# Performance work log

Hardware: AMD Instinct MI355X
Metric: run time of the kernel (lower is better)

The kernel has to match this reference:

```python
import jax, jax.numpy as jnp
import numpy as np

B = 64
L_IN = 4001
L_CONV = 998  # (4001-10)//4 + 1
D = 1000
EPS = 1e-5


def _convlin(x, cw, cb, lw, lb):
    # x: (B,1,4001), cw: (1,1,10), lw: (1000,998)
    y = jax.lax.conv_general_dilated(
        x, cw, window_strides=(4,), padding='VALID',
        dimension_numbers=('NCH', 'OIH', 'NCH')) + cb[None, :, None]  # (B,1,998)
    y = y @ lw.T + lb  # (B,1,1000)
    return jax.nn.relu(y)


def setup_inputs() -> dict:
    key = jax.random.key(0)
    ks = jax.random.split(key, 24)
    f32 = jnp.float32
    inp = {
        'x': jax.random.normal(ks[0], (B, 1, L_IN), dtype=f32),
        'bn_gamma': jnp.ones((L_IN,), f32),
        'bn_beta': jnp.zeros((L_IN,), f32),
        'bn_mean': jax.random.normal(ks[1], (L_IN,), f32) * 0.1,
        'bn_var': jax.random.uniform(ks[2], (L_IN,), f32, 0.5, 1.5),
        'conv_w_q': jax.random.normal(ks[3], (1, 1, 10), f32) * 0.3,
        'conv_b_q': jax.random.normal(ks[4], (1,), f32) * 0.1,
        'lin_w_q': jax.random.normal(ks[5], (D, L_CONV), f32) * (1.0 / np.sqrt(L_CONV)),
        'lin_b_q': jax.random.normal(ks[6], (D,), f32) * 0.02,
        'conv_w_k': jax.random.normal(ks[7], (1, 1, 10), f32) * 0.3,
        'conv_b_k': jax.random.normal(ks[8], (1,), f32) * 0.1,
        'lin_w_k': jax.random.normal(ks[9], (D, L_CONV), f32) * (1.0 / np.sqrt(L_CONV)),
        'lin_b_k': jax.random.normal(ks[10], (D,), f32) * 0.02,
        'conv_w_v': jax.random.normal(ks[11], (1, 1, 10), f32) * 0.3,
        'conv_b_v': jax.random.normal(ks[12], (1,), f32) * 0.1,
        'lin_w_v': jax.random.normal(ks[13], (D, L_CONV), f32) * (1.0 / np.sqrt(L_CONV)),
        'lin_b_v': jax.random.normal(ks[14], (D,), f32) * 0.02,
        'in_proj_w': jax.random.normal(ks[15], (3, 1), f32),
        'in_proj_b': jax.random.normal(ks[16], (3,), f32) * 0.02,
        'out_proj_w': jax.random.normal(ks[17], (1, 1), f32),
        'out_proj_b': jax.random.normal(ks[18], (1,), f32) * 0.02,
        'out_w': jax.random.normal(ks[19], (D, D), f32) * (1.0 / np.sqrt(D)),
        'out_b': jax.random.normal(ks[20], (D,), f32) * 0.02,
    }
    return inp


def reference(x, bn_gamma, bn_beta, bn_mean, bn_var,
              conv_w_q, conv_b_q, lin_w_q, lin_b_q,
              conv_w_k, conv_b_k, lin_w_k, lin_b_k,
              conv_w_v, conv_b_v, lin_w_v, lin_b_v,
              in_proj_w, in_proj_b, out_proj_w, out_proj_b,
              out_w, out_b):
    # BatchNorm1d over last dim (eval mode, running stats); x: (B,1,4001)
    xn = (x - bn_mean[None, None, :]) * jax.lax.rsqrt(bn_var[None, None, :] + EPS)
    xn = xn * bn_gamma[None, None, :] + bn_beta[None, None, :]

    Q = _convlin(xn, conv_w_q, conv_b_q, lin_w_q, lin_b_q)[:, 0, :]  # (B,1000)
    K = _convlin(xn, conv_w_k, conv_b_k, lin_w_k, lin_b_k)[:, 0, :]
    V = _convlin(xn, conv_w_v, conv_b_v, lin_w_v, lin_b_v)[:, 0, :]

    # MHA with embed_dim=1, num_heads=1 -> scalar in-projections, scale = 1
    q = Q * in_proj_w[0, 0] + in_proj_b[0]  # (B,1000)
    k = K * in_proj_w[1, 0] + in_proj_b[1]
    v = V * in_proj_w[2, 0] + in_proj_b[2]

    scores = q[:, :, None] * k[:, None, :]  # (B,1000,1000)
    attn = jax.nn.softmax(scores, axis=-1)
    ctx = jnp.einsum('bqk,bk->bq', attn, v)  # (B,1000)
    ctx = ctx * out_proj_w[0, 0] + out_proj_b[0]

    out = ctx[:, None, :] @ out_w.T + out_b  # (B,1,1000)
    return out
```

## Files before the change

kernel.cpp:

```cpp
#include <hip/hip_runtime.h>
#include <math.h>

#define NB 64
#define LIN 4001
#define LC 998
#define ND 1000
#define EPSBN 1e-5f

#define CKL 100
#define NCHL 10
#define CKO 96
#define NCHO 11

#define OFF_CONVT 0u
#define OFF_PP    191616u
#define OFF_CF    2157696u
#define OFF_OP    2221696u

__global__ __launch_bounds__(256) void k_bnconv(
    const float* __restrict__ x,
    const float* __restrict__ g, const float* __restrict__ be,
    const float* __restrict__ mu, const float* __restrict__ va,
    const float* __restrict__ cwq, const float* __restrict__ cbq,
    const float* __restrict__ cwk, const float* __restrict__ cbk,
    const float* __restrict__ cwv, const float* __restrict__ cbv,
    float* __restrict__ convT)
{
    int j = blockIdx.x * 256 + threadIdx.x;
    int b = blockIdx.y;
    if (j >= LC) return;
    const float* xb = x + (size_t)b * LIN + 4 * j;
    float aq = 0.f, ak = 0.f, av = 0.f;
#pragma unroll
    for (int t = 0; t < 10; ++t) {
        int i = 4 * j + t;
        float s  = g[i] * rsqrtf(va[i] + EPSBN);
        float xn = (xb[t] - mu[i]) * s + be[i];
        aq = fmaf(xn, cwq[t], aq);
        ak = fmaf(xn, cwk[t], ak);
        av = fmaf(xn, cwv[t], av);
    }
    convT[((size_t)0 * LC + j) * 64 + b] = aq + cbq[0];
    convT[((size_t)1 * LC + j) * 64 + b] = ak + cbk[0];
    convT[((size_t)2 * LC + j) * 64 + b] = av + cbv[0];
}

template <int CKT>
__device__ __forceinline__ void gemm_tile(
    const float* __restrict__ Asrc,
    const float* __restrict__ Brow,
    int ldB, int dgb, int j0, int jc,
    float* __restrict__ Pt,
    float* lds)
{
    constexpr int LDW = CKT + 1;
    constexpr int F2R = CKT / 2;
    float* ldsC = lds;
    float* ldsW = lds + CKT * 64;
    int tid  = threadIdx.x;
    int lane = tid & 63;
    int w    = tid >> 6;
    int b0   = (lane & 7) << 3;
    int d0   = (lane >> 3) << 3;

    {
        const float4* src = (const float4*)Asrc;
        float4* dst = (float4*)ldsC;
        int n = jc * 16;
        for (int t = tid; t < n; t += 256) dst[t] = src[t];
    }
    for (int idx = tid; idx < 64 * F2R; idx += 256) {
        int dd = idx / F2R, j2 = idx % F2R;
        int dg = dgb + dd;
        float2 v = make_float2(0.f, 0.f);
        if (dg < ND && 2 * j2 < jc)
            v = *(const float2*)(Brow + (size_t)dg * ldB + j0 + 2 * j2);
        ldsW[dd * LDW + 2 * j2]     = v.x;
        ldsW[dd * LDW + 2 * j2 + 1] = v.y;
    }
    __syncthreads();

    float acc[8][8];
#pragma unroll
    for (int i = 0; i < 8; ++i)
#pragma unroll
        for (int jx = 0; jx < 8; ++jx) acc[i][jx] = 0.f;

    int js = (jc * w) >> 2;
    int je = (jc * (w + 1)) >> 2;
#pragma unroll 2
    for (int jj = js; jj < je; ++jj) {
        float4 c0 = *(const float4*)(ldsC + jj * 64 + b0);
        float4 c1 = *(const float4*)(ldsC + jj * 64 + b0 + 4);
        float cv[8] = {c0.x, c0.y, c0.z, c0.w, c1.x, c1.y, c1.z, c1.w};
        float wv[8];
#pragma unroll
        for (int r = 0; r < 8; ++r) wv[r] = ldsW[(d0 + r) * LDW + jj];
#pragma unroll
        for (int i = 0; i < 8; ++i)
#pragma unroll
            for (int jx = 0; jx < 8; ++jx)
                acc[i][jx] = fmaf(cv[i], wv[jx], acc[i][jx]);
    }
    __syncthreads();

    for (int p = 0; p < 2; ++p) {
        float* red = lds + w * 2304;
#pragma unroll
        for (int i = 0; i < 8; ++i)
            *(float4*)(red + (b0 + i) * 36 + (d0 >> 1)) =
                make_float4(acc[i][4*p], acc[i][4*p+1], acc[i][4*p+2], acc[i][4*p+3]);
        __syncthreads();
        for (int t = tid; t < 512; t += 256) {
            int bb = t >> 3, gg = t & 7;
            int o = bb * 36 + 4 * gg;
            float4 a0 = *(const float4*)(lds + o);
            float4 a1 = *(const float4*)(lds + 2304 + o);
            float4 a2 = *(const float4*)(lds + 4608 + o);
            float4 a3 = *(const float4*)(lds + 6912 + o);
            float4 s;
            s.x = a0.x + a1.x + a2.x + a3.x;
            s.y = a0.y + a1.y + a2.y + a3.y;
            s.z = a0.z + a1.z + a2.z + a3.z;
            s.w = a0.w + a1.w + a2.w + a3.w;
            *(float4*)(Pt + bb * 64 + 8 * gg + 4 * p) = s;
        }
        __syncthreads();
    }
}

__global__ __launch_bounds__(256) void k_lin(
    const float* __restrict__ convT,
    const float* __restrict__ lwq, const float* __restrict__ lwk,
    const float* __restrict__ lwv,
    float* __restrict__ Pp)
{
    __shared__ float lds[12864];
    int dgb   = blockIdx.x * 64;
    int which = blockIdx.y;
    int chunk = blockIdx.z;
    int j0 = chunk * CKL;
    int jc = (LC - j0 < CKL) ? (LC - j0) : CKL;
    const float* lw = (which == 0) ? lwq : ((which == 1) ? lwk : lwv);
    const float* Asrc = convT + ((size_t)which * LC + j0) * 64;
    float* Pt = Pp + (((size_t)chunk * 3 + which) * 16 + blockIdx.x) * 4096;
    gemm_tile<CKL>(Asrc, lw, LC, dgb, j0, jc, Pt, lds);
}

__global__ __launch_bounds__(256) void k_actattn(
    const float* __restrict__ Pp,
    const float* __restrict__ lbq, const float* __restrict__ lbk,
    const float* __restrict__ lbv,
    const float* __restrict__ ipw, const float* __restrict__ ipb,
    const float* __restrict__ opw, const float* __restrict__ opb,
    float* __restrict__ cfT)
{
    __shared__ float ldsKV[2048];
    __shared__ float rmax[4];
    __shared__ float rmin[4];
    int tid = threadIdx.x;
    int iq  = blockIdx.x;
    int b   = blockIdx.y;
    int w   = tid >> 6;

    for (int i = tid; i < ND; i += 256) {
        int ig  = i >> 6;
        int off = (i & 63) | (b << 6);
        float s1 = 0.f, s2 = 0.f;
#pragma unroll
        for (int c = 0; c < NCHL; ++c) {
            size_t base = (((size_t)c * 3 + 1) * 16 + ig) * 4096 + off;
            s1 += Pp[base];
            s2 += Pp[base + 16 * 4096];
        }
        ldsKV[2 * i]     = fmaxf(s1 + lbk[i], 0.f) * ipw[1] + ipb[1];
        ldsKV[2 * i + 1] = fmaxf(s2 + lbv[i], 0.f) * ipw[2] + ipb[2];
    }
    int  i   = iq * 250 + tid;
    bool act = (tid < 250);
    float qi = 0.f;
    if (act) {
        int ig  = i >> 6;
        int off = (i & 63) | (b << 6);
        float s0 = 0.f;
#pragma unroll
        for (int c = 0; c < NCHL; ++c)
            s0 += Pp[(((size_t)c * 3) * 16 + ig) * 4096 + off];
        qi = fmaxf(s0 + lbq[i], 0.f) * ipw[0] + ipb[0];
    }
    __syncthreads();

    const float2* kv2 = (const float2*)ldsKV;
    float km = -INFINITY, kn = INFINITY;
    for (int idx = tid; idx < ND; idx += 256) {
        float2 f = kv2[idx];
        km = fmaxf(km, f.x);
        kn = fminf(kn, f.x);
    }
#pragma unroll
    for (int off = 1; off < 64; off <<= 1) {
        km = fmaxf(km, __shfl_xor(km, off));
        kn = fminf(kn, __shfl_xor(kn, off));
    }
    if ((tid & 63) == 0) { rmax[w] = km; rmin[w] = kn; }
    __syncthreads();
    km = fmaxf(fmaxf(rmax[0], rmax[1]), fmaxf(rmax[2], rmax[3]));
    kn = fminf(fminf(rmin[0], rmin[1]), fminf(rmin[2], rmin[3]));

    float m = (qi >= 0.f) ? qi * km : qi * kn;
    float den = 0.f, num = 0.f;
#pragma unroll 4
    for (int j = 0; j < ND; ++j) {
        float2 f = kv2[j];
        float e  = __expf(fmaf(qi, f.x, -m));
        den += e;
        num = fmaf(e, f.y, num);
    }
    if (act)
        cfT[(size_t)i * 64 + b] = (num / den) * opw[0] + opb[0];
}

__global__ __launch_bounds__(256) void k_out(
    const float* __restrict__ cfT, const float* __restrict__ W,
    float* __restrict__ Op)
{
    __shared__ float lds[12352];
    int egb   = blockIdx.x * 64;
    int chunk = blockIdx.y;
    int j0 = chunk * CKO;
    int jc = (ND - j0 < CKO) ? (ND - j0) : CKO;
    const float* Asrc = cfT + (size_t)j0 * 64;
    float* Pt = Op + ((size_t)chunk * 16 + blockIdx.x) * 4096;
    gemm_tile<CKO>(Asrc, W, ND, egb, j0, jc, Pt, lds);
}

__global__ __launch_bounds__(256) void k_fin(
    const float* __restrict__ Op, const float* __restrict__ outb,
    float* __restrict__ out)
{
    int e = blockIdx.x * 256 + threadIdx.x;
    int b = blockIdx.y;
    if (e >= ND) return;
    float s = outb[e];
    size_t cell = ((size_t)(e >> 6)) * 4096 + (b << 6) + (e & 63);
    for (int c = 0; c < NCHO; ++c)
        s += Op[(size_t)c * 16 * 4096 + cell];
    out[(size_t)b * ND + e] = s;
}

extern "C" void kernel_launch(void* const* d_in, const int* in_sizes, int n_in,
                              void* d_out, int out_size, void* d_ws, size_t ws_size,
                              hipStream_t stream)
{
    const float* x    = (const float*)d_in[0];
    const float* g    = (const float*)d_in[1];
    const float* be   = (const float*)d_in[2];
    const float* mu   = (const float*)d_in[3];
    const float* va   = (const float*)d_in[4];
    const float* cwq  = (const float*)d_in[5];
    const float* cbq  = (const float*)d_in[6];
    const float* lwq  = (const float*)d_in[7];
    const float* lbq  = (const float*)d_in[8];
    const float* cwk  = (const float*)d_in[9];
    const float* cbk  = (const float*)d_in[10];
    const float* lwk  = (const float*)d_in[11];
    const float* lbk  = (const float*)d_in[12];
    const float* cwv  = (const float*)d_in[13];
    const float* cbv  = (const float*)d_in[14];
    const float* lwv  = (const float*)d_in[15];
    const float* lbv  = (const float*)d_in[16];
    const float* ipw  = (const float*)d_in[17];
    const float* ipb  = (const float*)d_in[18];
    const float* opw  = (const float*)d_in[19];
    const float* opb  = (const float*)d_in[20];
    const float* W    = (const float*)d_in[21];
    const float* outb = (const float*)d_in[22];

    float* ws    = (float*)d_ws;
    float* convT = ws + OFF_CONVT;
    float* Pp    = ws + OFF_PP;
    float* cfT   = ws + OFF_CF;
    float* Op    = ws + OFF_OP;
    float* out   = (float*)d_out;

    k_bnconv <<<dim3(4, 64), 256, 0, stream>>>(x, g, be, mu, va,
                                               cwq, cbq, cwk, cbk, cwv, cbv, convT);
    k_lin    <<<dim3(16, 3, NCHL), 256, 0, stream>>>(convT, lwq, lwk, lwv, Pp);
    k_actattn<<<dim3(4, 64), 256, 0, stream>>>(Pp, lbq, lbk, lbv,
                                               ipw, ipb, opw, opb, cfT);
    k_out    <<<dim3(16, NCHO), 256, 0, stream>>>(cfT, W, Op);
    k_fin    <<<dim3(4, 64), 256, 0, stream>>>(Op, outb, out);
}
```

Baseline: 178.1 us.

## Replace split-K partial buffers with atomic accumulation and drop final reduction kernel

```diff
diff --git a/kernel.cpp b/kernel.cpp
--- a/kernel.cpp
+++ b/kernel.cpp
@@ -9,13 +9,13 @@
 
 #define CKL 100
 #define NCHL 10
-#define CKO 96
-#define NCHO 11
+#define CKO 50
+#define NCHO 20
 
 #define OFF_CONVT 0u
-#define OFF_PP    191616u
-#define OFF_CF    2157696u
-#define OFF_OP    2221696u
+#define OFF_Q     191616u
+#define OFF_KV    255616u
+#define OFF_CF    386688u
 
 __global__ __launch_bounds__(256) void k_bnconv(
     const float* __restrict__ x,
@@ -24,25 +24,39 @@
     const float* __restrict__ cwq, const float* __restrict__ cbq,
     const float* __restrict__ cwk, const float* __restrict__ cbk,
     const float* __restrict__ cwv, const float* __restrict__ cbv,
-    float* __restrict__ convT)
-{
-    int j = blockIdx.x * 256 + threadIdx.x;
-    int b = blockIdx.y;
-    if (j >= LC) return;
-    const float* xb = x + (size_t)b * LIN + 4 * j;
-    float aq = 0.f, ak = 0.f, av = 0.f;
-#pragma unroll
-    for (int t = 0; t < 10; ++t) {
-        int i = 4 * j + t;
-        float s  = g[i] * rsqrtf(va[i] + EPSBN);
-        float xn = (xb[t] - mu[i]) * s + be[i];
-        aq = fmaf(xn, cwq[t], aq);
-        ak = fmaf(xn, cwk[t], ak);
-        av = fmaf(xn, cwv[t], av);
-    }
-    convT[((size_t)0 * LC + j) * 64 + b] = aq + cbq[0];
-    convT[((size_t)1 * LC + j) * 64 + b] = ak + cbk[0];
-    convT[((size_t)2 * LC + j) * 64 + b] = av + cbv[0];
+    const float* __restrict__ lbq, const float* __restrict__ lbk,
+    const float* __restrict__ lbv, const float* __restrict__ outb,
+    float* __restrict__ convT,
+    float* __restrict__ q, float* __restrict__ kv, float* __restrict__ out)
+{
+    int tid = threadIdx.x;
+    int jt  = blockIdx.x;
+    int b   = blockIdx.y;
+
+    if (tid < 250) {
+        int e = jt * 250 + tid;
+        q[(size_t)b * ND + e] = lbq[e];
+        *(float2*)&kv[(size_t)b * 2048 + 2 * e] = make_float2(lbk[e], lbv[e]);
+        out[(size_t)b * ND + e] = outb[e];
+    }
+
+    int j = jt * 256 + tid;
+    if (j < LC) {
+        const float* xb = x + (size_t)b * LIN + 4 * j;
+        float aq = 0.f, ak = 0.f, av = 0.f;
+#pragma unroll
+        for (int t = 0; t < 10; ++t) {
+            int i = 4 * j + t;
+            float s  = g[i] * rsqrtf(va[i] + EPSBN);
+            float xn = (xb[t] - mu[i]) * s + be[i];
+            aq = fmaf(xn, cwq[t], aq);
+            ak = fmaf(xn, cwk[t], ak);
+            av = fmaf(xn, cwv[t], av);
+        }
+        convT[((size_t)0 * LC + j) * 64 + b] = aq + cbq[0];
+        convT[((size_t)1 * LC + j) * 64 + b] = ak + cbk[0];
+        convT[((size_t)2 * LC + j) * 64 + b] = av + cbv[0];
+    }
 }
 
 template <int CKT>
@@ -50,7 +64,7 @@
     const float* __restrict__ Asrc,
     const float* __restrict__ Brow,
     int ldB, int dgb, int j0, int jc,
-    float* __restrict__ Pt,
+    float* __restrict__ obase, int rowst, int cstr, int coff,
     float* lds)
 {
     constexpr int LDW = CKT + 1;
@@ -88,7 +102,6 @@
 
     int js = (jc * w) >> 2;
     int je = (jc * (w + 1)) >> 2;
-#pragma unroll 2
     for (int jj = js; jj < je; ++jj) {
         float4 c0 = *(const float4*)(ldsC + jj * 64 + b0);
         float4 c1 = *(const float4*)(ldsC + jj * 64 + b0 + 4);
@@ -123,7 +136,12 @@
             s.y = a0.y + a1.y + a2.y + a3.y;
             s.z = a0.z + a1.z + a2.z + a3.z;
             s.w = a0.w + a1.w + a2.w + a3.w;
-            *(float4*)(Pt + bb * 64 + 8 * gg + 4 * p) = s;
+            int col = dgb + 8 * gg + 4 * p;
+            float* row = obase + (size_t)bb * rowst;
+            if (col     < ND) atomicAdd(row + (size_t)(col    ) * cstr + coff, s.x);
+            if (col + 1 < ND) atomicAdd(row + (size_t)(col + 1) * cstr + coff, s.y);
+            if (col + 2 < ND) atomicAdd(row + (size_t)(col + 2) * cstr + coff, s.z);
+            if (col + 3 < ND) atomicAdd(row + (size_t)(col + 3) * cstr + coff, s.w);
         }
         __syncthreads();
     }
@@ -133,60 +151,48 @@
     const float* __restrict__ convT,
     const float* __restrict__ lwq, const float* __restrict__ lwk,
     const float* __restrict__ lwv,
-    float* __restrict__ Pp)
+    float* __restrict__ q, float* __restrict__ kv)
 {
     __shared__ float lds[12864];
-    int dgb   = blockIdx.x * 64;
+    int dgx   = blockIdx.x;
     int which = blockIdx.y;
     int chunk = blockIdx.z;
     int j0 = chunk * CKL;
     int jc = (LC - j0 < CKL) ? (LC - j0) : CKL;
     const float* lw = (which == 0) ? lwq : ((which == 1) ? lwk : lwv);
     const float* Asrc = convT + ((size_t)which * LC + j0) * 64;
-    float* Pt = Pp + (((size_t)chunk * 3 + which) * 16 + blockIdx.x) * 4096;
-    gemm_tile<CKL>(Asrc, lw, LC, dgb, j0, jc, Pt, lds);
-}
-
-__global__ __launch_bounds__(256) void k_actattn(
-    const float* __restrict__ Pp,
-    const float* __restrict__ lbq, const float* __restrict__ lbk,
-    const float* __restrict__ lbv,
+    float* obase; int rowst, cstr, coff;
+    if (which == 0) { obase = q;  rowst = ND;   cstr = 1; coff = 0; }
+    else            { obase = kv; rowst = 2048; cstr = 2; coff = which - 1; }
+    gemm_tile<CKL>(Asrc, lw, LC, dgx * 64, j0, jc, obase, rowst, cstr, coff, lds);
+}
+
+__global__ __launch_bounds__(256) void k_attn(
+    const float* __restrict__ q, const float* __restrict__ kv,
     const float* __restrict__ ipw, const float* __restrict__ ipb,
     const float* __restrict__ opw, const float* __restrict__ opb,
     float* __restrict__ cfT)
 {
     __shared__ float ldsKV[2048];
+    __shared__ float sden[256];
+    __shared__ float snum[256];
     __shared__ float rmax[4];
     __shared__ float rmin[4];
     int tid = threadIdx.x;
-    int iq  = blockIdx.x;
     int b   = blockIdx.y;
     int w   = tid >> 6;
-
-    for (int i = tid; i < ND; i += 256) {
-        int ig  = i >> 6;
-        int off = (i & 63) | (b << 6);
-        float s1 = 0.f, s2 = 0.f;
-#pragma unroll
-        for (int c = 0; c < NCHL; ++c) {
-            size_t base = (((size_t)c * 3 + 1) * 16 + ig) * 4096 + off;
-            s1 += Pp[base];
-            s2 += Pp[base + 16 * 4096];
+    int ii  = tid & 63;
+    int i   = blockIdx.x * 64 + ii;
+
+    {
+        const float2* src = (const float2*)(kv + (size_t)b * 2048);
+        float2* dst = (float2*)ldsKV;
+        float w1 = ipw[1], b1 = ipb[1], w2 = ipw[2], b2 = ipb[2];
+        for (int t = tid; t < 1024; t += 256) {
+            float2 rv = src[t];
+            dst[t] = make_float2(fmaf(fmaxf(rv.x, 0.f), w1, b1),
+                                 fmaf(fmaxf(rv.y, 0.f), w2, b2));
         }
-        ldsKV[2 * i]     = fmaxf(s1 + lbk[i], 0.f) * ipw[1] + ipb[1];
-        ldsKV[2 * i + 1] = fmaxf(s2 + lbv[i], 0.f) * ipw[2] + ipb[2];
-    }
-    int  i   = iq * 250 + tid;
-    bool act = (tid < 250);
-    float qi = 0.f;
-    if (act) {
-        int ig  = i >> 6;
-        int off = (i & 63) | (b << 6);
-        float s0 = 0.f;
-#pragma unroll
-        for (int c = 0; c < NCHL; ++c)
-            s0 += Pp[(((size_t)c * 3) * 16 + ig) * 4096 + off];
-        qi = fmaxf(s0 + lbq[i], 0.f) * ipw[0] + ipb[0];
     }
     __syncthreads();
 
@@ -202,50 +208,46 @@
         km = fmaxf(km, __shfl_xor(km, off));
         kn = fminf(kn, __shfl_xor(kn, off));
     }
-    if ((tid & 63) == 0) { rmax[w] = km; rmin[w] = kn; }
+    if (ii == 0) { rmax[w] = km; rmin[w] = kn; }
     __syncthreads();
     km = fmaxf(fmaxf(rmax[0], rmax[1]), fmaxf(rmax[2], rmax[3]));
     kn = fminf(fminf(rmin[0], rmin[1]), fminf(rmin[2], rmin[3]));
 
+    float qi = 0.f;
+    if (i < ND)
+        qi = fmaf(fmaxf(q[(size_t)b * ND + i], 0.f), ipw[0], ipb[0]);
     float m = (qi >= 0.f) ? qi * km : qi * kn;
+
+    int jb = w * 250;
     float den = 0.f, num = 0.f;
-#pragma unroll 4
-    for (int j = 0; j < ND; ++j) {
-        float2 f = kv2[j];
+#pragma unroll 2
+    for (int jl = 0; jl < 250; ++jl) {
+        float2 f = kv2[jb + jl];
         float e  = __expf(fmaf(qi, f.x, -m));
         den += e;
         num = fmaf(e, f.y, num);
     }
-    if (act)
-        cfT[(size_t)i * 64 + b] = (num / den) * opw[0] + opb[0];
+    sden[tid] = den;
+    snum[tid] = num;
+    __syncthreads();
+    if (w == 0 && i < ND) {
+        float dt = sden[ii] + sden[64 + ii] + sden[128 + ii] + sden[192 + ii];
+        float nt = snum[ii] + snum[64 + ii] + snum[128 + ii] + snum[192 + ii];
+        cfT[(size_t)i * 64 + b] = (nt / dt) * opw[0] + opb[0];
+    }
 }
 
 __global__ __launch_bounds__(256) void k_out(
     const float* __restrict__ cfT, const float* __restrict__ W,
-    float* __restrict__ Op)
-{
-    __shared__ float lds[12352];
-    int egb   = blockIdx.x * 64;
+    float* __restrict__ out)
+{
+    __shared__ float lds[9216];
+    int dgx   = blockIdx.x;
     int chunk = blockIdx.y;
     int j0 = chunk * CKO;
     int jc = (ND - j0 < CKO) ? (ND - j0) : CKO;
     const float* Asrc = cfT + (size_t)j0 * 64;
-    float* Pt = Op + ((size_t)chunk * 16 + blockIdx.x) * 4096;
-    gemm_tile<CKO>(Asrc, W, ND, egb, j0, jc, Pt, lds);
-}
-
-__global__ __launch_bounds__(256) void k_fin(
-    const float* __restrict__ Op, const float* __restrict__ outb,
-    float* __restrict__ out)
-{
-    int e = blockIdx.x * 256 + threadIdx.x;
-    int b = blockIdx.y;
-    if (e >= ND) return;
-    float s = outb[e];
-    size_t cell = ((size_t)(e >> 6)) * 4096 + (b << 6) + (e & 63);
-    for (int c = 0; c < NCHO; ++c)
-        s += Op[(size_t)c * 16 * 4096 + cell];
-    out[(size_t)b * ND + e] = s;
+    gemm_tile<CKO>(Asrc, W, ND, dgx * 64, j0, jc, out, ND, 1, 0, lds);
 }
 
 extern "C" void kernel_launch(void* const* d_in, const int* in_sizes, int n_in,
@@ -278,16 +280,16 @@
 
     float* ws    = (float*)d_ws;
     float* convT = ws + OFF_CONVT;
-    float* Pp    = ws + OFF_PP;
+    float* q     = ws + OFF_Q;
+    float* kv    = ws + OFF_KV;
     float* cfT   = ws + OFF_CF;
-    float* Op    = ws + OFF_OP;
     float* out   = (float*)d_out;
 
-    k_bnconv <<<dim3(4, 64), 256, 0, stream>>>(x, g, be, mu, va,
-                                               cwq, cbq, cwk, cbk, cwv, cbv, convT);
-    k_lin    <<<dim3(16, 3, NCHL), 256, 0, stream>>>(convT, lwq, lwk, lwv, Pp);
-    k_actattn<<<dim3(4, 64), 256, 0, stream>>>(Pp, lbq, lbk, lbv,
-                                               ipw, ipb, opw, opb, cfT);
-    k_out    <<<dim3(16, NCHO), 256, 0, stream>>>(cfT, W, Op);
-    k_fin    <<<dim3(4, 64), 256, 0, stream>>>(Op, outb, out);
-}
+    k_bnconv<<<dim3(4, 64), 256, 0, stream>>>(x, g, be, mu, va,
+                                              cwq, cbq, cwk, cbk, cwv, cbv,
+                                              lbq, lbk, lbv, outb,
+                                              convT, q, kv, out);
+    k_lin   <<<dim3(16, 3, NCHL), 256, 0, stream>>>(convT, lwq, lwk, lwv, q, kv);
+    k_attn  <<<dim3(16, 64), 256, 0, stream>>>(q, kv, ipw, ipb, opw, opb, cfT);
+    k_out   <<<dim3(16, NCHO), 256, 0, stream>>>(cfT, W, out);
+}
```

New measurement: 280.6 us. 1.58x slower.
